# Kernel optimization log

Measured on AMD Instinct MI355X. Metric: run time of the kernel, lower is better.

## Reference

```python
import jax, jax.numpy as jnp
import numpy as np

B, C, D, N, NCLS = 2048, 96, 384, 200000, 10
LN_EPS = 1e-5


def setup_inputs() -> dict:
    key = jax.random.key(0)
    ks = jax.random.split(key, 16)
    s = 0.05  # keep squared-distance logits in a sane range
    inp = {
        'k': jax.random.normal(ks[0], (B, D), jnp.float32) * s,
        'context_idx': jax.random.randint(ks[1], (B, C), 0, N),
        'candidate_embeddings': jax.random.normal(ks[2], (N, D), jnp.float32) * s,
        'candidate_y': jax.random.randint(ks[3], (N,), 0, NCLS),
        # learned params
        'label_emb': jax.random.normal(ks[4], (NCLS, D), jnp.float32) * 0.02,
        'ln_g': jnp.ones((D,), jnp.float32),
        'ln_b': jnp.zeros((D,), jnp.float32),
        'kp_w1': jax.random.normal(ks[5], (D, D), jnp.float32) * (1.0 / np.sqrt(D)),
        'kp_b1': jnp.zeros((D,), jnp.float32),
        'kp_w2': jax.random.normal(ks[6], (D, D), jnp.float32) * (1.0 / np.sqrt(D)),
        'kp_b2': jnp.zeros((D,), jnp.float32),
        'pw1': jax.random.normal(ks[7], (D, D), jnp.float32) * (1.0 / np.sqrt(D)),
        'pb1': jnp.zeros((D,), jnp.float32),
        'pw2': jax.random.normal(ks[8], (D, NCLS), jnp.float32) * (1.0 / np.sqrt(D)),
        'pb2': jnp.zeros((NCLS,), jnp.float32),
    }
    return inp


def reference(k, context_idx, candidate_embeddings, candidate_y,
              label_emb, ln_g, ln_b, kp_w1, kp_b1, kp_w2, kp_b2,
              pw1, pb1, pw2, pb2):
    # gather context (irregular access): [B, C, D], [B, C]
    context_k = candidate_embeddings[context_idx]
    context_y = candidate_y[context_idx]

    # negative squared distance via kernel trick: -|k|^2 + 2 k.ck - |ck|^2
    sim = (-jnp.sum(k * k, axis=-1, keepdims=True)
           + 2.0 * jnp.einsum('bd,bcd->bc', k, context_k)
           - jnp.sum(context_k * context_k, axis=-1))  # [B, C]
    probs = jax.nn.softmax(sim, axis=-1)  # dropout is identity in eval mode

    context_y_emb = label_emb[context_y]  # [B, C, D]

    # key_proj: LayerNorm -> Linear -> SiLU -> Linear, residual (d_main==n_out)
    def key_proj(x):
        mu = jnp.mean(x, axis=-1, keepdims=True)
        var = jnp.mean(jnp.square(x - mu), axis=-1, keepdims=True)
        h = (x - mu) * jax.lax.rsqrt(var + LN_EPS) * ln_g + ln_b
        h = jax.nn.silu(h @ kp_w1 + kp_b1)
        h = h @ kp_w2 + kp_b2
        return x + h

    # Abl == -1 branch: values = label_emb + key_proj(k - context_k)
    values = context_y_emb + key_proj(k[:, None, :] - context_k)  # [B, C, D]

    # probs[:, None] @ values -> weighted sum over context
    context_x = jnp.einsum('bc,bcd->bd', probs, values)
    x = k + context_x

    # predictor MLP (no residual: d_main != n_classes)
    h = jax.nn.silu(x @ pw1 + pb1)
    y = h @ pw2 + pb2
    return y
```

## Files before the change

kernel.cpp:

```cpp
#include <hip/hip_runtime.h>
#include <hip/hip_bf16.h>

#define BB   2048
#define CC   96
#define DD   384
#define NCLSS 10
#define AS_STRIDE 392

typedef __attribute__((ext_vector_type(8))) __bf16 bf16x8;
typedef __attribute__((ext_vector_type(4))) float  floatx4;
typedef unsigned int  uint32;
typedef unsigned short ushort16;
typedef __attribute__((ext_vector_type(4))) uint32 uintx4;

__device__ __forceinline__ float bflo(uint32 u){ return __uint_as_float(u << 16); }
__device__ __forceinline__ float bfhi(uint32 u){ return __uint_as_float(u & 0xffff0000u); }
__device__ __forceinline__ float bf1(ushort16 s){ return __uint_as_float(((uint32)s) << 16); }
__device__ __forceinline__ ushort16 f2bf(float f){
  uint32 u = __float_as_uint(f);
  return (ushort16)((u + 0x7fffu + ((u >> 16) & 1u)) >> 16);
}
__device__ __forceinline__ uint32 pk2bf(float lo, float hi){
  uint32 r;
  asm("v_cvt_pk_bf16_f32 %0, %1, %2" : "=v"(r) : "v"(lo), "v"(hi));
  return r;
}
__device__ __forceinline__ float fast_sig(float h){
  float e, rc;
  asm("v_exp_f32 %0, %1" : "=v"(e) : "v"(h * -1.44269504089f));
  float d = 1.f + e;
  asm("v_rcp_f32 %0, %1" : "=v"(rc) : "v"(d));
  return rc;
}
__device__ __forceinline__ int probe_f32(const void* lng_raw){
  return (((const uint32*)lng_raw)[0] == 0x3F800000u) ? 1 : 0;
}
__device__ __forceinline__ float ld1(const void* p, size_t i, int isf32){
  return isf32 ? ((const float*)p)[i] : bf1(((const ushort16*)p)[i]);
}

__global__ __launch_bounds__(256) void k_canon(
    const void* w1, const void* w2, const void* pw1,
    const void* lng, const void* lnb, const void* b1,
    ushort16* __restrict__ wW1T, ushort16* __restrict__ wW2T,
    ushort16* __restrict__ wPW1T,
    float* __restrict__ sconst, float* __restrict__ tconst)
{
  int isf32 = probe_f32(lng);
  if (blockIdx.x >= 432) {
    __shared__ float sred[8][32], tred[8][32];
    int bid = blockIdx.x - 432;
    int nl = threadIdx.x & 31, jl = threadIdx.x >> 5;
    int n = bid * 32 + nl;
    float s = 0.f, tt = 0.f;
    for (int j = jl; j < DD; j += 8) {
      float w = ld1(w1, (size_t)j * DD + n, isf32);
      s  += ld1(lng, j, isf32) * w;
      tt += ld1(lnb, j, isf32) * w;
    }
    sred[jl][nl] = s; tred[jl][nl] = tt;
    __syncthreads();
    if (jl == 0) {
      #pragma unroll
      for (int r = 1; r < 8; r++) { s += sred[r][nl]; tt += tred[r][nl]; }
      sconst[n] = s;
      tconst[n] = tt + ld1(b1, n, isf32);
    }
    return;
  }
  int m  = blockIdx.x / 144;
  int t  = blockIdx.x % 144;
  int tr = t / 12, tc = t % 12;
  const void* src = (m == 0) ? w1 : (m == 1) ? w2 : pw1;
  ushort16* dst   = (m == 0) ? wW1T : (m == 1) ? wW2T : wPW1T;
  __shared__ float tile[32][33];
  int tx = threadIdx.x & 31, ty = threadIdx.x >> 5;
  #pragma unroll
  for (int p = 0; p < 4; p++)
    tile[p*8 + ty][tx] = ld1(src, (size_t)(tr*32 + p*8 + ty) * DD + tc*32 + tx, isf32);
  __syncthreads();
  float gmul = (m == 0) ? ld1(lng, tr*32 + tx, isf32) : 1.f;
  #pragma unroll
  for (int p = 0; p < 4; p++)
    dst[(size_t)(tc*32 + p*8 + ty) * DD + tr*32 + tx] = f2bf(tile[tx][p*8 + ty] * gmul);
}

__global__ __launch_bounds__(512, 4) void k_fused(
    const void* kptr, const int* __restrict__ cidx,
    const void* cand, const int* __restrict__ cy,
    const void* lng,
    const ushort16* __restrict__ w1t,
    const float* __restrict__ sconst, const float* __restrict__ tconst,
    float* __restrict__ wxpre, float* __restrict__ wpl, float* __restrict__ wsum)
{
  int isf32 = probe_f32(lng);
  int b = blockIdx.x;
  int tid = threadIdx.x, wave = tid >> 6, lane = tid & 63;
  int t = lane & 15, kq = lane >> 4;
  __shared__ __align__(16) char AsB[96 * 768];
  __shared__ __align__(16) float ksh[DD];
  __shared__ float sims[CC], probs[CC], rsigv[CC], rmuv[CC];
  __shared__ float plbuf[NCLSS], xacc[DD];

  if (tid < NCLSS) plbuf[tid] = 0.f;
  if (tid < DD)    xacc[tid]  = 0.f;

  int c  = wave * 16 + t;
  int swz = (c & 7) << 4;
  int idx = 0;
  uintx4  ckr[12];
  floatx4 crf[12];

  if (wave < 6) {
    idx = cidx[b * CC + c];
    if (!isf32) {
      const uintx4* cp = (const uintx4*)((const ushort16*)cand + (size_t)idx * DD);
      #pragma unroll
      for (int kt = 0; kt < 12; kt++) ckr[kt] = cp[kt*4 + kq];
    } else {
      const float* cf = (const float*)cand + (size_t)idx * DD;
      #pragma unroll
      for (int q = 0; q < 6; q++) {
        int j0 = q*32 + kq*8;
        crf[2*q]   = *(const floatx4*)(cf + j0);
        crf[2*q+1] = *(const floatx4*)(cf + j0 + 4);
      }
    }
  } else {
    int q = tid - 384;
    #pragma unroll
    for (int r = 0; r < 3; r++)
      ksh[q + 128*r] = ld1(kptr, (size_t)b * DD + q + 128*r, isf32);
  }
  __builtin_amdgcn_sched_barrier(0);
  asm volatile("s_waitcnt lgkmcnt(0)\n\ts_barrier" ::: "memory");

  float s1 = 0.f, s2 = 0.f;
  if (wave < 6) {
    if (!isf32) {
      #pragma unroll
      for (int kt = 0; kt < 12; kt++) {
        int j0 = kt*32 + kq*8;
        floatx4 ka = *(const floatx4*)&ksh[j0];
        floatx4 kb = *(const floatx4*)&ksh[j0+4];
        float kk[8] = {ka[0],ka[1],ka[2],ka[3],kb[0],kb[1],kb[2],kb[3]};
        float ck[8] = {bflo(ckr[kt][0]),bfhi(ckr[kt][0]),bflo(ckr[kt][1]),bfhi(ckr[kt][1]),
                       bflo(ckr[kt][2]),bfhi(ckr[kt][2]),bflo(ckr[kt][3]),bfhi(ckr[kt][3])};
        float d[8];
        #pragma unroll
        for (int j = 0; j < 8; j++) { d[j] = kk[j] - ck[j]; s1 += d[j]; s2 += d[j]*d[j]; }
        uintx4 vv = { pk2bf(d[0],d[1]), pk2bf(d[2],d[3]), pk2bf(d[4],d[5]), pk2bf(d[6],d[7]) };
        *(uintx4*)(AsB + ((c * 768 + kt * 64 + kq * 16) ^ swz)) = vv;
      }
    } else {
      const float* cf = (const float*)cand + (size_t)idx * DD;
      #pragma unroll
      for (int h = 0; h < 2; h++) {
        if (h == 1) {
          #pragma unroll
          for (int q = 0; q < 6; q++) {
            int j0 = (6+q)*32 + kq*8;
            crf[2*q]   = *(const floatx4*)(cf + j0);
            crf[2*q+1] = *(const floatx4*)(cf + j0 + 4);
          }
        }
        #pragma unroll
        for (int q = 0; q < 6; q++) {
          int kt = h*6 + q;
          int j0 = kt*32 + kq*8;
          floatx4 ka = *(const floatx4*)&ksh[j0];
          floatx4 kb = *(const floatx4*)&ksh[j0+4];
          float kk[8] = {ka[0],ka[1],ka[2],ka[3],kb[0],kb[1],kb[2],kb[3]};
          float ck[8] = {crf[2*q][0],crf[2*q][1],crf[2*q][2],crf[2*q][3],
                         crf[2*q+1][0],crf[2*q+1][1],crf[2*q+1][2],crf[2*q+1][3]};
          float d[8];
          #pragma unroll
          for (int j = 0; j < 8; j++) { d[j] = kk[j] - ck[j]; s1 += d[j]; s2 += d[j]*d[j]; }
          uintx4 vv = { pk2bf(d[0],d[1]), pk2bf(d[2],d[3]), pk2bf(d[4],d[5]), pk2bf(d[6],d[7]) };
          *(uintx4*)(AsB + ((c * 768 + kt * 64 + kq * 16) ^ swz)) = vv;
        }
      }
    }
    s1 += __shfl_xor(s1, 16); s2 += __shfl_xor(s2, 16);
    s1 += __shfl_xor(s1, 32); s2 += __shfl_xor(s2, 32);
    float mu = s1 * (1.f/DD), var = s2 * (1.f/DD) - mu*mu;
    float rsig = rsqrtf(var + 1e-5f);
    if (kq == 0) { sims[c] = -s2; rsigv[c] = rsig; rmuv[c] = rsig * mu; }
  }
  __syncthreads();

  if (wave == 0) {
    float v0 = sims[lane];
    float v1 = (lane < 32) ? sims[lane + 64] : -1e30f;
    float mx = fmaxf(v0, v1);
    #pragma unroll
    for (int m = 32; m; m >>= 1) mx = fmaxf(mx, __shfl_xor(mx, m));
    float e0 = __expf(v0 - mx);
    float e1 = (lane < 32) ? __expf(v1 - mx) : 0.f;
    float s = e0 + e1;
    #pragma unroll
    for (int m = 32; m; m >>= 1) s += __shfl_xor(s, m);
    float inv = 1.f / s;
    probs[lane] = e0 * inv;
    if (lane < 32) probs[lane + 64] = e1 * inv;
  }
  __syncthreads();

  if (tid < CC) atomicAdd(&plbuf[cy[cidx[b * CC + tid]]], probs[tid]);
  {
    float T0=0,T1=0,T2=0,T3=0,T4=0,T5=0;
    #pragma unroll
    for (int i = 0; i < 12; i++) {
      int cc = wave * 12 + i;
      float p = probs[cc];
      const char* rp = AsB + cc * 768;
      int sz = (cc & 7) << 4;
      uint32 a0 = *(const uint32*)(rp + ((lane*12 + 0) ^ sz));
      uint32 a1 = *(const uint32*)(rp + ((lane*12 + 4) ^ sz));
      uint32 a2 = *(const uint32*)(rp + ((lane*12 + 8) ^ sz));
      T0 += p*bflo(a0); T1 += p*bfhi(a0); T2 += p*bflo(a1);
      T3 += p*bfhi(a1); T4 += p*bflo(a2); T5 += p*bfhi(a2);
    }
    int j0 = lane * 6;
    atomicAdd(&xacc[j0+0], T0); atomicAdd(&xacc[j0+1], T1);
    atomicAdd(&xacc[j0+2], T2); atomicAdd(&xacc[j0+3], T3);
    atomicAdd(&xacc[j0+4], T4); atomicAdd(&xacc[j0+5], T5);
  }
  __syncthreads();

  if (tid < DD)
    wxpre[(size_t)b * DD + tid] = ksh[tid] + xacc[tid];
  if (tid < NCLSS) wpl[b * NCLSS + tid] = plbuf[tid];

  int col = lane & 15, quad = lane >> 4;
  int n0 = wave * 48;
  floatx4 acc[6][3];
  #pragma unroll
  for (int i = 0; i < 6; i++)
    #pragma unroll
    for (int j = 0; j < 3; j++) acc[i][j] = (floatx4)0.f;

  const ushort16* wbase = w1t + (size_t)(n0 + col) * DD + quad * 8;
  bf16x8 bcur[3];
  #pragma unroll
  for (int tn = 0; tn < 3; tn++)
    bcur[tn] = *(const bf16x8*)(wbase + (size_t)tn * 16 * DD);
  #pragma unroll 1
  for (int kt = 0; kt < 12; kt++) {
    bf16x8 bnxt[3] = { (bf16x8)0, (bf16x8)0, (bf16x8)0 };
    if (kt < 11) {
      #pragma unroll
      for (int tn = 0; tn < 3; tn++)
        bnxt[tn] = *(const bf16x8*)(wbase + (size_t)tn * 16 * DD + (kt+1) * 32);
    }
    #pragma unroll
    for (int tm = 0; tm < 6; tm++) {
      int r = tm*16 + col;
      bf16x8 afrag = *(const bf16x8*)(AsB + ((r * 768 + kt*64 + quad*16) ^ ((r & 7) << 4)));
      #pragma unroll
      for (int tn = 0; tn < 3; tn++)
        acc[tm][tn] = __builtin_amdgcn_mfma_f32_16x16x32_bf16(afrag, bcur[tn], acc[tm][tn], 0, 0, 0);
    }
    #pragma unroll
    for (int tn = 0; tn < 3; tn++) bcur[tn] = bnxt[tn];
  }

  float snv[3], tnv[3], val[3];
  #pragma unroll
  for (int tn = 0; tn < 3; tn++) {
    int n = n0 + tn*16 + col;
    snv[tn] = sconst[n]; tnv[tn] = tconst[n]; val[tn] = 0.f;
  }
  #pragma unroll
  for (int tm = 0; tm < 6; tm++) {
    float pr[4], rs[4], rm[4];
    #pragma unroll
    for (int r = 0; r < 4; r++) {
      int row = tm*16 + quad*4 + r;
      pr[r] = probs[row]; rs[r] = rsigv[row]; rm[r] = rmuv[row];
    }
    #pragma unroll
    for (int tn = 0; tn < 3; tn++) {
      #pragma unroll
      for (int r = 0; r < 4; r++) {
        float h = rs[r] * acc[tm][tn][r] - rm[r] * snv[tn] + tnv[tn];
        val[tn] += pr[r] * (h * fast_sig(h));
      }
    }
  }
  #pragma unroll
  for (int tn = 0; tn < 3; tn++) {
    float v = val[tn];
    v += __shfl_xor(v, 16);
    v += __shfl_xor(v, 32);
    if (quad == 0) wsum[(size_t)b * DD + n0 + tn*16 + col] = v;
  }
}

__global__ __launch_bounds__(512) void k_final(
    const float* __restrict__ wxpre, const float* __restrict__ wsum,
    const float* __restrict__ wpl, const void* lemb,
    const ushort16* __restrict__ w2t, const void* b2,
    const ushort16* __restrict__ pw1t, const void* pb1,
    const void* pw2, const void* pb2,
    const void* lng_raw, void* out)
{
  int isf32 = probe_f32(lng_raw);
  int b0 = blockIdx.x * 8;
  int tid = threadIdx.x, wave = tid >> 6, lane = tid & 63;
  int cn = lane & 15, quad = lane >> 4;
  __shared__ __align__(16) ushort16 As[16 * AS_STRIDE];
  __shared__ float hbuf[8][AS_STRIDE];
  __shared__ float lembsh[NCLSS * DD];
  __shared__ float plsh[8][NCLSS];
  __shared__ float part[480];

  for (int e = tid; e < 16 * AS_STRIDE; e += 512) {
    int r = e / AS_STRIDE, j = e - r * AS_STRIDE;
    ushort16 v = (ushort16)0;
    if (r < 8 && j < DD) v = f2bf(wsum[(size_t)(b0 + r) * DD + j]);
    As[e] = v;
  }
  for (int e = tid; e < NCLSS * DD; e += 512) lembsh[e] = ld1(lemb, e, isf32);
  if (tid < 80) plsh[tid / NCLSS][tid % NCLSS] = wpl[(b0 + tid / NCLSS) * NCLSS + tid % NCLSS];
  __syncthreads();

  int n0 = wave * 48;
  floatx4 acc[3];
  #pragma unroll
  for (int j = 0; j < 3; j++) acc[j] = (floatx4)0.f;
  const ushort16* wb2 = w2t + (size_t)(n0 + cn) * DD + quad * 8;
  #pragma unroll 2
  for (int kt = 0; kt < 12; kt++) {
    bf16x8 afrag = *(const bf16x8*)(As + cn * AS_STRIDE + kt*32 + quad*8);
    #pragma unroll
    for (int tn = 0; tn < 3; tn++) {
      bf16x8 bfrag = *(const bf16x8*)(wb2 + (size_t)tn * 16 * DD + kt * 32);
      acc[tn] = __builtin_amdgcn_mfma_f32_16x16x32_bf16(afrag, bfrag, acc[tn], 0, 0, 0);
    }
  }
  float xv[3][4];
  #pragma unroll
  for (int tn = 0; tn < 3; tn++) {
    int n = n0 + tn*16 + cn;
    float bb = ld1(b2, n, isf32);
    #pragma unroll
    for (int r = 0; r < 4; r++) {
      int row = quad*4 + r;
      if (row < 8) {
        float v = acc[tn][r] + bb + wxpre[(size_t)(b0 + row) * DD + n];
        #pragma unroll
        for (int l = 0; l < NCLSS; l++) v += plsh[row][l] * lembsh[l * DD + n];
        xv[tn][r] = v;
      }
    }
  }
  __syncthreads();
  #pragma unroll
  for (int tn = 0; tn < 3; tn++) {
    int n = n0 + tn*16 + cn;
    #pragma unroll
    for (int r = 0; r < 4; r++) {
      int row = quad*4 + r;
      if (row < 8) As[row * AS_STRIDE + n] = f2bf(xv[tn][r]);
    }
  }
  __syncthreads();

  floatx4 acc2[3];
  #pragma unroll
  for (int j = 0; j < 3; j++) acc2[j] = (floatx4)0.f;
  const ushort16* wbp = pw1t + (size_t)(n0 + cn) * DD + quad * 8;
  #pragma unroll 2
  for (int kt = 0; kt < 12; kt++) {
    bf16x8 afrag = *(const bf16x8*)(As + cn * AS_STRIDE + kt*32 + quad*8);
    #pragma unroll
    for (int tn = 0; tn < 3; tn++) {
      bf16x8 bfrag = *(const bf16x8*)(wbp + (size_t)tn * 16 * DD + kt * 32);
      acc2[tn] = __builtin_amdgcn_mfma_f32_16x16x32_bf16(afrag, bfrag, acc2[tn], 0, 0, 0);
    }
  }
  #pragma unroll
  for (int tn = 0; tn < 3; tn++) {
    int n = n0 + tn*16 + cn;
    float bb = ld1(pb1, n, isf32);
    #pragma unroll
    for (int r = 0; r < 4; r++) {
      int row = quad*4 + r;
      if (row < 8) {
        float h = acc2[tn][r] + bb;
        hbuf[row][n] = h / (1.f + __expf(-h));
      }
    }
  }
  __syncthreads();

  if (tid < 480) {
    int r = tid / 60, rem = tid % 60, n = rem / 6, s = rem % 6;
    float pp = 0.f;
    int jb = s * 64;
    #pragma unroll 8
    for (int jj = 0; jj < 64; jj++) {
      int j = jb + jj;
      pp += hbuf[r][j] * ld1(pw2, (size_t)j * NCLSS + n, isf32);
    }
    part[tid] = pp;
  }
  __syncthreads();
  if (tid < 80) {
    int r = tid / NCLSS, n = tid % NCLSS;
    float y = ld1(pb2, n, isf32);
    #pragma unroll
    for (int s = 0; s < 6; s++) y += part[r*60 + n*6 + s];
    size_t o = (size_t)(b0 + r) * NCLSS + n;
    if (isf32) ((float*)out)[o] = y;
    else       ((ushort16*)out)[o] = f2bf(y);
  }
}

extern "C" void kernel_launch(void* const* d_in, const int* in_sizes, int n_in,
                              void* d_out, int out_size, void* d_ws, size_t ws_size,
                              hipStream_t stream) {
  const void* kptr = d_in[0];
  const int*  cidx = (const int*)d_in[1];
  const void* cand = d_in[2];
  const int*  cy   = (const int*)d_in[3];
  const void* lemb = d_in[4];
  const void* lng  = d_in[5];
  const void* lnb  = d_in[6];
  const void* w1   = d_in[7];
  const void* b1   = d_in[8];
  const void* w2   = d_in[9];
  const void* b2   = d_in[10];
  const void* pw1  = d_in[11];
  const void* pb1  = d_in[12];
  const void* pw2  = d_in[13];
  const void* pb2  = d_in[14];

  char* ws = (char*)d_ws;
  ushort16* wW1T   = (ushort16*)(ws);
  ushort16* wW2T   = (ushort16*)(ws + 294912);
  ushort16* wPW1T  = (ushort16*)(ws + 589824);
  float*    wxpre  = (float*)   (ws + 884736);
  float*    wpl    = (float*)   (ws + 4030464);
  float*    wsum   = (float*)   (ws + 4112384);
  float*    sconst = (float*)   (ws + 7258112);
  float*    tconst = (float*)   (ws + 7259648);

  k_canon<<<444, 256, 0, stream>>>(w1, w2, pw1, lng, lnb, b1,
                                   wW1T, wW2T, wPW1T, sconst, tconst);
  k_fused<<<BB, 512, 0, stream>>>(kptr, cidx, cand, cy, lng, wW1T,
                                  sconst, tconst, wxpre, wpl, wsum);
  k_final<<<256, 512, 0, stream>>>(wxpre, wsum, wpl, lemb, wW2T, b2,
                                   wPW1T, pb1, pw2, pb2, lng, d_out);
}
```

Before: 583.2 us.

## Make fused kernel persistent with double-buffered prefetch of next batch row's gather

```diff
diff --git a/kernel.cpp b/kernel.cpp
--- a/kernel.cpp
+++ b/kernel.cpp
@@ -31,6 +31,9 @@
   float d = 1.f + e;
   asm("v_rcp_f32 %0, %1" : "=v"(rc) : "v"(d));
   return rc;
+}
+__device__ __forceinline__ void barl(){
+  asm volatile("s_waitcnt lgkmcnt(0)\n\ts_barrier" ::: "memory");
 }
 __device__ __forceinline__ int probe_f32(const void* lng_raw){
   return (((const uint32*)lng_raw)[0] == 0x3F800000u) ? 1 : 0;
@@ -85,7 +88,7 @@
     dst[(size_t)(tc*32 + p*8 + ty) * DD + tr*32 + tx] = f2bf(tile[tx][p*8 + ty] * gmul);
 }
 
-__global__ __launch_bounds__(512, 4) void k_fused(
+__global__ __launch_bounds__(512, 2) void k_fused(
     const void* kptr, const int* __restrict__ cidx,
     const void* cand, const int* __restrict__ cy,
     const void* lng,
@@ -94,31 +97,35 @@
     float* __restrict__ wxpre, float* __restrict__ wpl, float* __restrict__ wsum)
 {
   int isf32 = probe_f32(lng);
-  int b = blockIdx.x;
   int tid = threadIdx.x, wave = tid >> 6, lane = tid & 63;
   int t = lane & 15, kq = lane >> 4;
-  __shared__ __align__(16) char AsB[96 * 768];
-  __shared__ __align__(16) float ksh[DD];
-  __shared__ float sims[CC], probs[CC], rsigv[CC], rmuv[CC];
+  __shared__ __align__(16) char  AsB[2][96 * 768];
+  __shared__ __align__(16) float ksh[2][DD];
+  __shared__ float sims[CC], probs[CC];
+  __shared__ float rsigv[2][CC], rmuv[2][CC];
   __shared__ float plbuf[NCLSS], xacc[DD];
 
   if (tid < NCLSS) plbuf[tid] = 0.f;
   if (tid < DD)    xacc[tid]  = 0.f;
 
-  int c  = wave * 16 + t;
+  int c   = wave * 16 + t;
   int swz = (c & 7) << 4;
-  int idx = 0;
+  int col = lane & 15, quad = lane >> 4;
+  int n0  = wave * 48;
+
   uintx4  ckr[12];
   floatx4 crf[12];
-
-  if (wave < 6) {
-    idx = cidx[b * CC + c];
+  int idxn = 0;
+  float kr0 = 0.f, kr1 = 0.f, kr2 = 0.f;
+
+  auto issue = [&](int bg){
+    idxn = cidx[bg * CC + c];
     if (!isf32) {
-      const uintx4* cp = (const uintx4*)((const ushort16*)cand + (size_t)idx * DD);
+      const uintx4* cp = (const uintx4*)((const ushort16*)cand + (size_t)idxn * DD);
       #pragma unroll
       for (int kt = 0; kt < 12; kt++) ckr[kt] = cp[kt*4 + kq];
     } else {
-      const float* cf = (const float*)cand + (size_t)idx * DD;
+      const float* cf = (const float*)cand + (size_t)idxn * DD;
       #pragma unroll
       for (int q = 0; q < 6; q++) {
         int j0 = q*32 + kq*8;
@@ -126,34 +133,38 @@
         crf[2*q+1] = *(const floatx4*)(cf + j0 + 4);
       }
     }
-  } else {
+  };
+  auto kissue = [&](int bg){
     int q = tid - 384;
-    #pragma unroll
-    for (int r = 0; r < 3; r++)
-      ksh[q + 128*r] = ld1(kptr, (size_t)b * DD + q + 128*r, isf32);
-  }
-  __builtin_amdgcn_sched_barrier(0);
-  asm volatile("s_waitcnt lgkmcnt(0)\n\ts_barrier" ::: "memory");
-
-  float s1 = 0.f, s2 = 0.f;
-  if (wave < 6) {
+    kr0 = ld1(kptr, (size_t)bg*DD + q,       isf32);
+    kr1 = ld1(kptr, (size_t)bg*DD + q + 128, isf32);
+    kr2 = ld1(kptr, (size_t)bg*DD + q + 256, isf32);
+  };
+  auto kwrite = [&](int buf){
+    int q = tid - 384;
+    ksh[buf][q] = kr0; ksh[buf][q+128] = kr1; ksh[buf][q+256] = kr2;
+  };
+  auto process = [&](int buf){
+    float s1 = 0.f, s2 = 0.f;
+    char* dst = AsB[buf];
     if (!isf32) {
       #pragma unroll
       for (int kt = 0; kt < 12; kt++) {
         int j0 = kt*32 + kq*8;
-        floatx4 ka = *(const floatx4*)&ksh[j0];
-        floatx4 kb = *(const floatx4*)&ksh[j0+4];
-        float kk[8] = {ka[0],ka[1],ka[2],ka[3],kb[0],kb[1],kb[2],kb[3]};
-        float ck[8] = {bflo(ckr[kt][0]),bfhi(ckr[kt][0]),bflo(ckr[kt][1]),bfhi(ckr[kt][1]),
-                       bflo(ckr[kt][2]),bfhi(ckr[kt][2]),bflo(ckr[kt][3]),bfhi(ckr[kt][3])};
+        floatx4 ka = *(const floatx4*)&ksh[buf][j0];
+        floatx4 kb = *(const floatx4*)&ksh[buf][j0+4];
         float d[8];
-        #pragma unroll
-        for (int j = 0; j < 8; j++) { d[j] = kk[j] - ck[j]; s1 += d[j]; s2 += d[j]*d[j]; }
+        d[0]=ka[0]-bflo(ckr[kt][0]); d[1]=ka[1]-bfhi(ckr[kt][0]);
+        d[2]=ka[2]-bflo(ckr[kt][1]); d[3]=ka[3]-bfhi(ckr[kt][1]);
+        d[4]=kb[0]-bflo(ckr[kt][2]); d[5]=kb[1]-bfhi(ckr[kt][2]);
+        d[6]=kb[2]-bflo(ckr[kt][3]); d[7]=kb[3]-bfhi(ckr[kt][3]);
+        #pragma unroll
+        for (int j = 0; j < 8; j++) { s1 += d[j]; s2 += d[j]*d[j]; }
         uintx4 vv = { pk2bf(d[0],d[1]), pk2bf(d[2],d[3]), pk2bf(d[4],d[5]), pk2bf(d[6],d[7]) };
-        *(uintx4*)(AsB + ((c * 768 + kt * 64 + kq * 16) ^ swz)) = vv;
+        *(uintx4*)(dst + ((c*768 + kt*64 + kq*16) ^ swz)) = vv;
       }
     } else {
-      const float* cf = (const float*)cand + (size_t)idx * DD;
+      const float* cf = (const float*)cand + (size_t)idxn * DD;
       #pragma unroll
       for (int h = 0; h < 2; h++) {
         if (h == 1) {
@@ -168,16 +179,16 @@
         for (int q = 0; q < 6; q++) {
           int kt = h*6 + q;
           int j0 = kt*32 + kq*8;
-          floatx4 ka = *(const floatx4*)&ksh[j0];
-          floatx4 kb = *(const floatx4*)&ksh[j0+4];
-          float kk[8] = {ka[0],ka[1],ka[2],ka[3],kb[0],kb[1],kb[2],kb[3]};
-          float ck[8] = {crf[2*q][0],crf[2*q][1],crf[2*q][2],crf[2*q][3],
-                         crf[2*q+1][0],crf[2*q+1][1],crf[2*q+1][2],crf[2*q+1][3]};
-          float d[8];
+          floatx4 ka = *(const floatx4*)&ksh[buf][j0];
+          floatx4 kb = *(const floatx4*)&ksh[buf][j0+4];
+          float d[8] = {ka[0]-crf[2*q][0], ka[1]-crf[2*q][1],
+                        ka[2]-crf[2*q][2], ka[3]-crf[2*q][3],
+                        kb[0]-crf[2*q+1][0], kb[1]-crf[2*q+1][1],
+                        kb[2]-crf[2*q+1][2], kb[3]-crf[2*q+1][3]};
           #pragma unroll
-          for (int j = 0; j < 8; j++) { d[j] = kk[j] - ck[j]; s1 += d[j]; s2 += d[j]*d[j]; }
+          for (int j = 0; j < 8; j++) { s1 += d[j]; s2 += d[j]*d[j]; }
           uintx4 vv = { pk2bf(d[0],d[1]), pk2bf(d[2],d[3]), pk2bf(d[4],d[5]), pk2bf(d[6],d[7]) };
-          *(uintx4*)(AsB + ((c * 768 + kt * 64 + kq * 16) ^ swz)) = vv;
+          *(uintx4*)(dst + ((c*768 + kt*64 + kq*16) ^ swz)) = vv;
         }
       }
     }
@@ -185,115 +196,137 @@
     s1 += __shfl_xor(s1, 32); s2 += __shfl_xor(s2, 32);
     float mu = s1 * (1.f/DD), var = s2 * (1.f/DD) - mu*mu;
     float rsig = rsqrtf(var + 1e-5f);
-    if (kq == 0) { sims[c] = -s2; rsigv[c] = rsig; rmuv[c] = rsig * mu; }
-  }
-  __syncthreads();
-
-  if (wave == 0) {
-    float v0 = sims[lane];
-    float v1 = (lane < 32) ? sims[lane + 64] : -1e30f;
-    float mx = fmaxf(v0, v1);
-    #pragma unroll
-    for (int m = 32; m; m >>= 1) mx = fmaxf(mx, __shfl_xor(mx, m));
-    float e0 = __expf(v0 - mx);
-    float e1 = (lane < 32) ? __expf(v1 - mx) : 0.f;
-    float s = e0 + e1;
-    #pragma unroll
-    for (int m = 32; m; m >>= 1) s += __shfl_xor(s, m);
-    float inv = 1.f / s;
-    probs[lane] = e0 * inv;
-    if (lane < 32) probs[lane + 64] = e1 * inv;
-  }
-  __syncthreads();
-
-  if (tid < CC) atomicAdd(&plbuf[cy[cidx[b * CC + tid]]], probs[tid]);
+    if (kq == 0) { sims[c] = -s2; rsigv[buf][c] = rsig; rmuv[buf][c] = rsig*mu; }
+  };
+
+  int cur = 0;
   {
-    float T0=0,T1=0,T2=0,T3=0,T4=0,T5=0;
-    #pragma unroll
-    for (int i = 0; i < 12; i++) {
-      int cc = wave * 12 + i;
-      float p = probs[cc];
-      const char* rp = AsB + cc * 768;
-      int sz = (cc & 7) << 4;
-      uint32 a0 = *(const uint32*)(rp + ((lane*12 + 0) ^ sz));
-      uint32 a1 = *(const uint32*)(rp + ((lane*12 + 4) ^ sz));
-      uint32 a2 = *(const uint32*)(rp + ((lane*12 + 8) ^ sz));
-      T0 += p*bflo(a0); T1 += p*bfhi(a0); T2 += p*bflo(a1);
-      T3 += p*bfhi(a1); T4 += p*bflo(a2); T5 += p*bfhi(a2);
-    }
-    int j0 = lane * 6;
-    atomicAdd(&xacc[j0+0], T0); atomicAdd(&xacc[j0+1], T1);
-    atomicAdd(&xacc[j0+2], T2); atomicAdd(&xacc[j0+3], T3);
-    atomicAdd(&xacc[j0+4], T4); atomicAdd(&xacc[j0+5], T5);
-  }
-  __syncthreads();
-
-  if (tid < DD)
-    wxpre[(size_t)b * DD + tid] = ksh[tid] + xacc[tid];
-  if (tid < NCLSS) wpl[b * NCLSS + tid] = plbuf[tid];
-
-  int col = lane & 15, quad = lane >> 4;
-  int n0 = wave * 48;
-  floatx4 acc[6][3];
-  #pragma unroll
-  for (int i = 0; i < 6; i++)
-    #pragma unroll
-    for (int j = 0; j < 3; j++) acc[i][j] = (floatx4)0.f;
-
-  const ushort16* wbase = w1t + (size_t)(n0 + col) * DD + quad * 8;
-  bf16x8 bcur[3];
-  #pragma unroll
-  for (int tn = 0; tn < 3; tn++)
-    bcur[tn] = *(const bf16x8*)(wbase + (size_t)tn * 16 * DD);
-  #pragma unroll 1
-  for (int kt = 0; kt < 12; kt++) {
-    bf16x8 bnxt[3] = { (bf16x8)0, (bf16x8)0, (bf16x8)0 };
-    if (kt < 11) {
+    int b0 = blockIdx.x;
+    if (wave < 6) issue(b0);
+    else { kissue(b0); kwrite(0); }
+    barl();
+    if (wave < 6) process(0);
+    barl();
+  }
+
+  for (int it = 0; it < 8; it++) {
+    int b   = blockIdx.x + 256*it;
+    int nxt = cur ^ 1;
+    int pf  = (it < 7);
+    if (pf) {
+      int bn = blockIdx.x + 256*(it+1);
+      if (wave < 6) issue(bn); else kissue(bn);
+    }
+    __builtin_amdgcn_sched_barrier(0);
+    if (wave == 0) {
+      float v0 = sims[lane];
+      float v1 = (lane < 32) ? sims[lane + 64] : -1e30f;
+      float mx = fmaxf(v0, v1);
+      #pragma unroll
+      for (int m = 32; m; m >>= 1) mx = fmaxf(mx, __shfl_xor(mx, m));
+      float e0 = __expf(v0 - mx);
+      float e1 = (lane < 32) ? __expf(v1 - mx) : 0.f;
+      float s = e0 + e1;
+      #pragma unroll
+      for (int m = 32; m; m >>= 1) s += __shfl_xor(s, m);
+      float inv = 1.f / s;
+      probs[lane] = e0 * inv;
+      if (lane < 32) probs[lane + 64] = e1 * inv;
+    }
+    barl();
+    if (pf && wave >= 6) kwrite(nxt);
+    if (tid < CC) atomicAdd(&plbuf[cy[cidx[b * CC + tid]]], probs[tid]);
+    {
+      float T0=0,T1=0,T2=0,T3=0,T4=0,T5=0;
+      const char* bufc = AsB[cur];
+      #pragma unroll
+      for (int i = 0; i < 12; i++) {
+        int cc = wave * 12 + i;
+        float p = probs[cc];
+        const char* rp = bufc + cc * 768;
+        int sz = (cc & 7) << 4;
+        uint32 a0 = *(const uint32*)(rp + ((lane*12 + 0) ^ sz));
+        uint32 a1 = *(const uint32*)(rp + ((lane*12 + 4) ^ sz));
+        uint32 a2 = *(const uint32*)(rp + ((lane*12 + 8) ^ sz));
+        T0 += p*bflo(a0); T1 += p*bfhi(a0); T2 += p*bflo(a1);
+        T3 += p*bfhi(a1); T4 += p*bflo(a2); T5 += p*bfhi(a2);
+      }
+      int j0 = lane * 6;
+      atomicAdd(&xacc[j0+0], T0); atomicAdd(&xacc[j0+1], T1);
+      atomicAdd(&xacc[j0+2], T2); atomicAdd(&xacc[j0+3], T3);
+      atomicAdd(&xacc[j0+4], T4); atomicAdd(&xacc[j0+5], T5);
+    }
+    barl();
+    if (tid < DD) {
+      wxpre[(size_t)b * DD + tid] = ksh[cur][tid] + xacc[tid];
+      xacc[tid] = 0.f;
+    }
+    if (tid < NCLSS) { wpl[b * NCLSS + tid] = plbuf[tid]; plbuf[tid] = 0.f; }
+    {
+      floatx4 acc[6][3];
+      #pragma unroll
+      for (int i = 0; i < 6; i++)
+        #pragma unroll
+        for (int j = 0; j < 3; j++) acc[i][j] = (floatx4)0.f;
+      const ushort16* wbase = w1t + (size_t)(n0 + col) * DD + quad * 8;
+      const char* bufc = AsB[cur];
+      bf16x8 bcur[3];
       #pragma unroll
       for (int tn = 0; tn < 3; tn++)
-        bnxt[tn] = *(const bf16x8*)(wbase + (size_t)tn * 16 * DD + (kt+1) * 32);
-    }
-    #pragma unroll
-    for (int tm = 0; tm < 6; tm++) {
-      int r = tm*16 + col;
-      bf16x8 afrag = *(const bf16x8*)(AsB + ((r * 768 + kt*64 + quad*16) ^ ((r & 7) << 4)));
-      #pragma unroll
-      for (int tn = 0; tn < 3; tn++)
-        acc[tm][tn] = __builtin_amdgcn_mfma_f32_16x16x32_bf16(afrag, bcur[tn], acc[tm][tn], 0, 0, 0);
-    }
-    #pragma unroll
-    for (int tn = 0; tn < 3; tn++) bcur[tn] = bnxt[tn];
-  }
-
-  float snv[3], tnv[3], val[3];
-  #pragma unroll
-  for (int tn = 0; tn < 3; tn++) {
-    int n = n0 + tn*16 + col;
-    snv[tn] = sconst[n]; tnv[tn] = tconst[n]; val[tn] = 0.f;
-  }
-  #pragma unroll
-  for (int tm = 0; tm < 6; tm++) {
-    float pr[4], rs[4], rm[4];
-    #pragma unroll
-    for (int r = 0; r < 4; r++) {
-      int row = tm*16 + quad*4 + r;
-      pr[r] = probs[row]; rs[r] = rsigv[row]; rm[r] = rmuv[row];
-    }
-    #pragma unroll
-    for (int tn = 0; tn < 3; tn++) {
-      #pragma unroll
-      for (int r = 0; r < 4; r++) {
-        float h = rs[r] * acc[tm][tn][r] - rm[r] * snv[tn] + tnv[tn];
-        val[tn] += pr[r] * (h * fast_sig(h));
-      }
-    }
-  }
-  #pragma unroll
-  for (int tn = 0; tn < 3; tn++) {
-    float v = val[tn];
-    v += __shfl_xor(v, 16);
-    v += __shfl_xor(v, 32);
-    if (quad == 0) wsum[(size_t)b * DD + n0 + tn*16 + col] = v;
+        bcur[tn] = *(const bf16x8*)(wbase + (size_t)tn * 16 * DD);
+      #pragma unroll 1
+      for (int kt = 0; kt < 12; kt++) {
+        bf16x8 bnxt[3] = { (bf16x8)0, (bf16x8)0, (bf16x8)0 };
+        if (kt < 11) {
+          #pragma unroll
+          for (int tn = 0; tn < 3; tn++)
+            bnxt[tn] = *(const bf16x8*)(wbase + (size_t)tn * 16 * DD + (kt+1) * 32);
+        }
+        #pragma unroll
+        for (int tm = 0; tm < 6; tm++) {
+          int r = tm*16 + col;
+          bf16x8 afrag = *(const bf16x8*)(bufc + ((r * 768 + kt*64 + quad*16) ^ ((r & 7) << 4)));
+          #pragma unroll
+          for (int tn = 0; tn < 3; tn++)
+            acc[tm][tn] = __builtin_amdgcn_mfma_f32_16x16x32_bf16(afrag, bcur[tn], acc[tm][tn], 0, 0, 0);
+        }
+        #pragma unroll
+        for (int tn = 0; tn < 3; tn++) bcur[tn] = bnxt[tn];
+      }
+      float snv[3], tnv[3], val[3];
+      #pragma unroll
+      for (int tn = 0; tn < 3; tn++) {
+        int n = n0 + tn*16 + col;
+        snv[tn] = sconst[n]; tnv[tn] = tconst[n]; val[tn] = 0.f;
+      }
+      #pragma unroll
+      for (int tm = 0; tm < 6; tm++) {
+        float pr[4], rs[4], rm[4];
+        #pragma unroll
+        for (int r = 0; r < 4; r++) {
+          int row = tm*16 + quad*4 + r;
+          pr[r] = probs[row]; rs[r] = rsigv[cur][row]; rm[r] = rmuv[cur][row];
+        }
+        #pragma unroll
+        for (int tn = 0; tn < 3; tn++) {
+          #pragma unroll
+          for (int r = 0; r < 4; r++) {
+            float h = rs[r] * acc[tm][tn][r] - rm[r] * snv[tn] + tnv[tn];
+            val[tn] += pr[r] * (h * fast_sig(h));
+          }
+        }
+      }
+      #pragma unroll
+      for (int tn = 0; tn < 3; tn++) {
+        float v = val[tn];
+        v += __shfl_xor(v, 16);
+        v += __shfl_xor(v, 32);
+        if (quad == 0) wsum[(size_t)b * DD + n0 + tn*16 + col] = v;
+      }
+    }
+    if (pf && wave < 6) process(nxt);
+    barl();
+    cur = nxt;
   }
 }
 
@@ -449,8 +482,8 @@
 
   k_canon<<<444, 256, 0, stream>>>(w1, w2, pw1, lng, lnb, b1,
                                    wW1T, wW2T, wPW1T, sconst, tconst);
-  k_fused<<<BB, 512, 0, stream>>>(kptr, cidx, cand, cy, lng, wW1T,
-                                  sconst, tconst, wxpre, wpl, wsum);
+  k_fused<<<256, 512, 0, stream>>>(kptr, cidx, cand, cy, lng, wW1T,
+                                   sconst, tconst, wxpre, wpl, wsum);
   k_final<<<256, 512, 0, stream>>>(wxpre, wsum, wpl, lemb, wW2T, b2,
                                    wPW1T, pb1, pw2, pb2, lng, d_out);
 }
```

Result: slower. 677.8 us (+16.2%).
